# Kernel optimization log

Measured on AMD Instinct MI355X. Metric: run time of the kernel, lower is better.

Reference implementation:

```python
import jax, jax.numpy as jnp
import numpy as np

B, T, K = 512, 512, 128
START, STOP = K - 2, K - 1
NEG = -10000.0


def setup_inputs() -> dict:
    key = jax.random.key(0)
    k1, k2, k3, k4 = jax.random.split(key, 4)
    feats = jax.random.normal(k1, (B, T, K), dtype=jnp.float32)
    transitions = jax.random.normal(k2, (K, K), dtype=jnp.float32)
    # CRF.__init__ clamps transitions INTO the start tag and OUT of the stop tag
    transitions = transitions.at[START, :].set(NEG).at[:, STOP].set(NEG)
    tags = jax.random.randint(k3, (B, T), 0, K - 2, dtype=jnp.int32)
    lengths = jax.random.randint(k4, (B,), 1, T + 1, dtype=jnp.int32)
    return {"feats": feats, "transitions": transitions, "tags": tags, "lengths": lengths}


def _forward_alg(feats, trans, lengths):
    # feats: [B, T, K]
    Bb, Tt, Kk = feats.shape
    alpha0 = jnp.full((Bb, Kk), NEG, dtype=feats.dtype).at[:, START].set(0.0)

    def step(alpha, emit):
        # tag_var[b, j, k] = emit[b, j] + trans[j, k] + alpha[b, k]
        tag_var = emit[:, :, None] + trans[None, :, :] + alpha[:, None, :]
        new = jax.nn.logsumexp(tag_var, axis=2)  # stable max + log-sum-exp
        return new, new

    _, alphas = jax.lax.scan(step, alpha0, jnp.swapaxes(feats, 0, 1))  # [T, B, K]
    alphas_all = jnp.concatenate([alpha0[None], alphas], axis=0)       # [T+1, B, K]
    # pick forward_var at position lengths[b] (original indexes [b, lens_[b], :])
    fv = alphas_all[lengths, jnp.arange(Bb)]                            # [B, K]
    terminal = fv + trans[STOP][None, :]
    return jax.nn.logsumexp(terminal, axis=1)                           # [B]


def _score_sentence(feats, trans, tags, lengths):
    Bb, Tt, Kk = feats.shape
    pos = jnp.arange(Tt)
    valid = pos[None, :] < lengths[:, None]                             # [B, T]
    # pad_stop_tags: tags with positions >= len replaced by STOP, then STOP appended
    tags_stop = jnp.where(valid, tags, STOP)
    pad_stop = jnp.concatenate(
        [tags_stop, jnp.full((Bb, 1), STOP, dtype=tags.dtype)], axis=1)  # [B, T+1]
    pad_start = jnp.concatenate(
        [jnp.full((Bb, 1), START, dtype=tags.dtype), tags], axis=1)     # [B, T+1]
    trans_terms = trans[pad_stop, pad_start]                            # [B, T+1]
    tmask = jnp.arange(Tt + 1)[None, :] <= lengths[:, None]             # i in [0, len]
    tscore = jnp.sum(jnp.where(tmask, trans_terms, 0.0), axis=1)
    emit = jnp.take_along_axis(feats, tags[:, :, None].astype(jnp.int32), axis=2)[:, :, 0]
    escore = jnp.sum(jnp.where(valid, emit, 0.0), axis=1)
    return tscore + escore                                              # [B]


def reference(feats, transitions, tags, lengths):
    forward_score = _forward_alg(feats, transitions, lengths)
    gold_score = _score_sentence(feats, transitions, tags, lengths)
    return jnp.mean(jnp.abs(forward_score - gold_score))
```

## Files before the change

### kernel.cpp

```cpp
#include <hip/hip_runtime.h>
#include <math.h>

#define KK 128
#define TT 512
#define BB 512
#define TAG_START 126
#define TAG_STOP 127

typedef float v4f __attribute__((ext_vector_type(4)));

#define XI(j) ((j) + (((j) >> 5) << 2))

template <int CTRL>
__device__ __forceinline__ float dpp_movf(float x) {
    return __int_as_float(
        __builtin_amdgcn_update_dpp(0, __float_as_int(x), CTRL, 0xF, 0xF, true));
}

#define STEP_BARRIER() asm volatile("s_waitcnt lgkmcnt(0)\n\ts_barrier" ::: "memory")


__global__ __launch_bounds__(512) void order_kernel(const int* __restrict__ lengths,
                                                    int* __restrict__ order) {
    __shared__ int L[BB];
    int tid = threadIdx.x;
    L[tid] = lengths[tid];
    __syncthreads();
    int mylen = L[tid];
    int r = 0;
    for (int i = 0; i < BB; i++) {
        int li = L[i];
        r += (li > mylen) || (li == mylen && i < tid);
    }
    order[r] = tid;
}

__global__ __launch_bounds__(512, 4) void fused_kernel(
    const float* __restrict__ feats, const float* __restrict__ trans,
    const int* __restrict__ tags, const int* __restrict__ lengths,
    const int* __restrict__ order,
    float* __restrict__ fwd_out, float* __restrict__ gold_out) {
    int tid = threadIdx.x;
    int w = tid >> 6;
    int l = tid & 63;

    if (blockIdx.x < BB) {
        int b = order[blockIdx.x];

        __shared__ __align__(16) float xs[2][160];
        __shared__ float As[2];
        __shared__ float redm[8], reds[8];

        int g = (l >> 4) & 3;
        int c = l & 15;
        bool b0 = (l & 1) != 0;
        bool b1 = (l & 2) != 0;
        int row_mine = 16 * w + 4 * g + 2 * (l & 1) + ((l >> 1) & 1);
        int xoff = 8 * c + 4 * (c >> 2);
        int xw = XI(row_mine);
        bool writer = (l & 12) == 0;

        v4f tv[8];
#pragma unroll
        for (int r = 0; r < 4; r++) {
            const float* tp = trans + (16 * w + 4 * g + r) * KK + 8 * c;
            asm volatile("global_load_dwordx4 %0, %1, off"
                         : "=v"(tv[2 * r]) : "v"(tp));
            asm volatile("global_load_dwordx4 %0, %1, off"
                         : "=v"(tv[2 * r + 1]) : "v"(tp + 4));
        }
        int len = lengths[b];
        const float* fbr = feats + (size_t)b * TT * KK + row_mine;
        asm volatile("s_waitcnt vmcnt(0)"
                     : "+v"(tv[0]), "+v"(tv[1]), "+v"(tv[2]), "+v"(tv[3]),
                       "+v"(tv[4]), "+v"(tv[5]), "+v"(tv[6]), "+v"(tv[7]));

        float Mj0, Mj1, Mj2, Mj3;
        {
            float m[4];
#pragma unroll
            for (int r = 0; r < 4; r++) {
                v4f aL = tv[2 * r], aH = tv[2 * r + 1];
                float mm = fmaxf(fmaxf(fmaxf(aL.x, aL.y), fmaxf(aL.z, aL.w)),
                                 fmaxf(fmaxf(aH.x, aH.y), fmaxf(aH.z, aH.w)));
#pragma unroll
                for (int off = 1; off <= 8; off <<= 1)
                    mm = fmaxf(mm, __shfl_xor(mm, off));
                m[r] = mm;
            }
            Mj0 = m[0]; Mj1 = m[1]; Mj2 = m[2]; Mj3 = m[3];
        }
        float Mj_mine = b0 ? (b1 ? Mj3 : Mj2) : (b1 ? Mj1 : Mj0);

        float Erow[32];
#pragma unroll
        for (int r = 0; r < 4; r++) {
            float mr = (r == 0) ? Mj0 : (r == 1) ? Mj1 : (r == 2) ? Mj2 : Mj3;
            Erow[8 * r + 0] = __expf(tv[2 * r].x - mr);
            Erow[8 * r + 1] = __expf(tv[2 * r].y - mr);
            Erow[8 * r + 2] = __expf(tv[2 * r].z - mr);
            Erow[8 * r + 3] = __expf(tv[2 * r].w - mr);
            Erow[8 * r + 4] = __expf(tv[2 * r + 1].x - mr);
            Erow[8 * r + 5] = __expf(tv[2 * r + 1].y - mr);
            Erow[8 * r + 6] = __expf(tv[2 * r + 1].z - mr);
            Erow[8 * r + 7] = __expf(tv[2 * r + 1].w - mr);
        }

        if (writer) xs[0][xw] = (row_mine == TAG_START) ? 1.0f : 0.0f;
        if (tid == 0) { As[0] = 0.f; As[1] = 0.f; }

        float alpha = 0.f, A = 0.f;
        float emb[8];
#pragma unroll
        for (int d = 0; d < 8; d++) {
            int tf = (d < len) ? d : (len - 1);
            emb[d] = fbr[(size_t)tf * KK];
        }
        __syncthreads();

        int tmax = (len + 7) & ~7;
        for (int t0 = 0; t0 < tmax; t0 += 8) {
#pragma unroll
            for (int d = 0; d < 8; d++) {
                int t = t0 + d;
                if (t < len) {
                    float em = emb[d];
                    int tf = (t + 8 < len) ? (t + 8) : (len - 1);
                    emb[d] = fbr[(size_t)tf * KK];

                    int cur = t & 1, nxt = cur ^ 1;
                    float Sn = As[nxt];
                    float fac = __expf(em + Mj_mine + A - Sn);
                    const v4f* xp = (const v4f*)(xs[cur] + xoff);
                    v4f xa = xp[0], xb = xp[1];
                    float a0 = 0.f, a1 = 0.f, a2 = 0.f, a3 = 0.f;
                    a0 = fmaf(Erow[0], xa.x, a0);  a0 = fmaf(Erow[1], xa.y, a0);
                    a0 = fmaf(Erow[2], xa.z, a0);  a0 = fmaf(Erow[3], xa.w, a0);
                    a0 = fmaf(Erow[4], xb.x, a0);  a0 = fmaf(Erow[5], xb.y, a0);
                    a0 = fmaf(Erow[6], xb.z, a0);  a0 = fmaf(Erow[7], xb.w, a0);
                    a1 = fmaf(Erow[8], xa.x, a1);  a1 = fmaf(Erow[9], xa.y, a1);
                    a1 = fmaf(Erow[10], xa.z, a1); a1 = fmaf(Erow[11], xa.w, a1);
                    a1 = fmaf(Erow[12], xb.x, a1); a1 = fmaf(Erow[13], xb.y, a1);
                    a1 = fmaf(Erow[14], xb.z, a1); a1 = fmaf(Erow[15], xb.w, a1);
                    a2 = fmaf(Erow[16], xa.x, a2); a2 = fmaf(Erow[17], xa.y, a2);
                    a2 = fmaf(Erow[18], xa.z, a2); a2 = fmaf(Erow[19], xa.w, a2);
                    a2 = fmaf(Erow[20], xb.x, a2); a2 = fmaf(Erow[21], xb.y, a2);
                    a2 = fmaf(Erow[22], xb.z, a2); a2 = fmaf(Erow[23], xb.w, a2);
                    a3 = fmaf(Erow[24], xa.x, a3); a3 = fmaf(Erow[25], xa.y, a3);
                    a3 = fmaf(Erow[26], xa.z, a3); a3 = fmaf(Erow[27], xa.w, a3);
                    a3 = fmaf(Erow[28], xb.x, a3); a3 = fmaf(Erow[29], xb.y, a3);
                    a3 = fmaf(Erow[30], xb.z, a3); a3 = fmaf(Erow[31], xb.w, a3);
                    float k0 = b0 ? a2 : a0;
                    float k1 = b0 ? a3 : a1;
                    float s0 = b0 ? a0 : a2;
                    float s1 = b0 ? a1 : a3;
                    k0 += dpp_movf<0xB1>(s0);
                    k1 += dpp_movf<0xB1>(s1);
                    float kk = b1 ? k1 : k0;
                    float ss = b1 ? k0 : k1;
                    kk += dpp_movf<0x4E>(ss);
                    kk += dpp_movf<0x124>(kk);
                    kk += dpp_movf<0x128>(kk);
                    if (writer) xs[nxt][xw] = kk * fac;
                    alpha = em + Mj_mine + A + __logf(kk);
                    if (tid == 0) As[cur] = alpha;
                    A = Sn;
                    STEP_BARRIER();
                }
            }
        }

        float term = writer ? (alpha + trans[TAG_STOP * KK + row_mine]) : -1e30f;
        float m = term;
#pragma unroll
        for (int off = 32; off >= 1; off >>= 1) m = fmaxf(m, __shfl_xor(m, off));
        float s = writer ? __expf(term - m) : 0.f;
#pragma unroll
        for (int off = 32; off >= 1; off >>= 1) s += __shfl_xor(s, off);
        if (l == 0) { redm[w] = m; reds[w] = s; }
        __syncthreads();
        if (tid == 0) {
            float M2 = redm[0];
            for (int i = 1; i < 8; i++) M2 = fmaxf(M2, redm[i]);
            float S2 = 0.f;
            for (int i = 0; i < 8; i++) S2 += reds[i] * __expf(redm[i] - M2);
            fwd_out[b] = M2 + __logf(S2);
        }
    } else {
        int b = blockIdx.x - BB;
        int len = lengths[b];
        const int* tg = tags + (size_t)b * TT;
        const float* fb = feats + (size_t)b * TT * KK;
        float acc = 0.f;
        for (int i = tid; i <= len; i += 512) {
            int from = (i == 0) ? TAG_START : tg[i - 1];
            int to = (i < len) ? tg[i] : TAG_STOP;
            acc += trans[to * KK + from];
        }
        for (int t = tid; t < len; t += 512)
            acc += fb[(size_t)t * KK + tg[t]];
        __shared__ float sred[8];
#pragma unroll
        for (int off = 32; off >= 1; off >>= 1) acc += __shfl_xor(acc, off);
        if ((tid & 63) == 0) sred[tid >> 6] = acc;
        __syncthreads();
        if (tid == 0) {
            float s = 0.f;
            for (int i = 0; i < 8; i++) s += sred[i];
            gold_out[b] = s;
        }
    }
}

__global__ __launch_bounds__(512) void final_kernel(const float* __restrict__ fwd_s,
                                                    const float* __restrict__ gold_s,
                                                    float* __restrict__ out) {
    int tid = threadIdx.x;
    float v = fabsf(fwd_s[tid] - gold_s[tid]);
#pragma unroll
    for (int off = 32; off >= 1; off >>= 1) v += __shfl_xor(v, off);
    __shared__ float sred[8];
    if ((tid & 63) == 0) sred[tid >> 6] = v;
    __syncthreads();
    if (tid == 0) {
        float s = 0.f;
        for (int i = 0; i < 8; i++) s += sred[i];
        out[0] = s / (float)BB;
    }
}

extern "C" void kernel_launch(void* const* d_in, const int* in_sizes, int n_in,
                              void* d_out, int out_size, void* d_ws, size_t ws_size,
                              hipStream_t stream) {
    const float* feats = (const float*)d_in[0];
    const float* trans = (const float*)d_in[1];
    const int* tags = (const int*)d_in[2];
    const int* lengths = (const int*)d_in[3];

    float* ws = (float*)d_ws;
    float* fwdv = ws;
    float* goldv = ws + BB;
    int* order = (int*)(ws + 2 * BB);

    order_kernel<<<1, 512, 0, stream>>>(lengths, order);
    fused_kernel<<<2 * BB, 512, 0, stream>>>(feats, trans, tags, lengths, order,
                                             fwdv, goldv);
    final_kernel<<<1, 512, 0, stream>>>(fwdv, goldv, (float*)d_out);
}
```

Before: 341.1 us.

## Use persistent blocks with atomic work queue and interleaved length ordering

```diff
diff --git a/kernel.cpp b/kernel.cpp
--- a/kernel.cpp
+++ b/kernel.cpp
@@ -21,9 +21,11 @@
 
 
 __global__ __launch_bounds__(512) void order_kernel(const int* __restrict__ lengths,
-                                                    int* __restrict__ order) {
+                                                    int* __restrict__ order,
+                                                    int* __restrict__ ctr) {
     __shared__ int L[BB];
     int tid = threadIdx.x;
+    if (tid == 0) *ctr = 0;
     L[tid] = lengths[tid];
     __syncthreads();
     int mylen = L[tid];
@@ -32,182 +34,193 @@
         int li = L[i];
         r += (li > mylen) || (li == mylen && i < tid);
     }
-    order[r] = tid;
+    int task = (r < BB / 2) ? (2 * r) : (2 * (BB - 1 - r) + 1);
+    order[task] = tid;
 }
 
 __global__ __launch_bounds__(512, 4) void fused_kernel(
     const float* __restrict__ feats, const float* __restrict__ trans,
     const int* __restrict__ tags, const int* __restrict__ lengths,
-    const int* __restrict__ order,
+    const int* __restrict__ order, int* __restrict__ ctr,
     float* __restrict__ fwd_out, float* __restrict__ gold_out) {
     int tid = threadIdx.x;
     int w = tid >> 6;
     int l = tid & 63;
 
-    if (blockIdx.x < BB) {
-        int b = order[blockIdx.x];
-
-        __shared__ __align__(16) float xs[2][160];
-        __shared__ float As[2];
-        __shared__ float redm[8], reds[8];
-
-        int g = (l >> 4) & 3;
-        int c = l & 15;
-        bool b0 = (l & 1) != 0;
-        bool b1 = (l & 2) != 0;
-        int row_mine = 16 * w + 4 * g + 2 * (l & 1) + ((l >> 1) & 1);
-        int xoff = 8 * c + 4 * (c >> 2);
-        int xw = XI(row_mine);
-        bool writer = (l & 12) == 0;
-
-        v4f tv[8];
+    __shared__ __align__(16) float xs[2][160];
+    __shared__ float As[2];
+    __shared__ float redm[8], reds[8];
+    __shared__ float sred[8];
+    __shared__ int task_s;
+
+    int g = (l >> 4) & 3;
+    int c = l & 15;
+    bool b0 = (l & 1) != 0;
+    bool b1 = (l & 2) != 0;
+    int row_mine = 16 * w + 4 * g + 2 * (l & 1) + ((l >> 1) & 1);
+    int xoff = 8 * c + 4 * (c >> 2);
+    int xw = XI(row_mine);
+    bool writer = (l & 12) == 0;
+
+    v4f tv[8];
+#pragma unroll
+    for (int r = 0; r < 4; r++) {
+        const float* tp = trans + (16 * w + 4 * g + r) * KK + 8 * c;
+        asm volatile("global_load_dwordx4 %0, %1, off"
+                     : "=v"(tv[2 * r]) : "v"(tp));
+        asm volatile("global_load_dwordx4 %0, %1, off"
+                     : "=v"(tv[2 * r + 1]) : "v"(tp + 4));
+    }
+    asm volatile("s_waitcnt vmcnt(0)"
+                 : "+v"(tv[0]), "+v"(tv[1]), "+v"(tv[2]), "+v"(tv[3]),
+                   "+v"(tv[4]), "+v"(tv[5]), "+v"(tv[6]), "+v"(tv[7]));
+
+    float Mj0, Mj1, Mj2, Mj3;
+    {
+        float m[4];
 #pragma unroll
         for (int r = 0; r < 4; r++) {
-            const float* tp = trans + (16 * w + 4 * g + r) * KK + 8 * c;
-            asm volatile("global_load_dwordx4 %0, %1, off"
-                         : "=v"(tv[2 * r]) : "v"(tp));
-            asm volatile("global_load_dwordx4 %0, %1, off"
-                         : "=v"(tv[2 * r + 1]) : "v"(tp + 4));
+            v4f aL = tv[2 * r], aH = tv[2 * r + 1];
+            float mm = fmaxf(fmaxf(fmaxf(aL.x, aL.y), fmaxf(aL.z, aL.w)),
+                             fmaxf(fmaxf(aH.x, aH.y), fmaxf(aH.z, aH.w)));
+#pragma unroll
+            for (int off = 1; off <= 8; off <<= 1)
+                mm = fmaxf(mm, __shfl_xor(mm, off));
+            m[r] = mm;
         }
-        int len = lengths[b];
-        const float* fbr = feats + (size_t)b * TT * KK + row_mine;
-        asm volatile("s_waitcnt vmcnt(0)"
-                     : "+v"(tv[0]), "+v"(tv[1]), "+v"(tv[2]), "+v"(tv[3]),
-                       "+v"(tv[4]), "+v"(tv[5]), "+v"(tv[6]), "+v"(tv[7]));
-
-        float Mj0, Mj1, Mj2, Mj3;
-        {
-            float m[4];
-#pragma unroll
-            for (int r = 0; r < 4; r++) {
-                v4f aL = tv[2 * r], aH = tv[2 * r + 1];
-                float mm = fmaxf(fmaxf(fmaxf(aL.x, aL.y), fmaxf(aL.z, aL.w)),
-                                 fmaxf(fmaxf(aH.x, aH.y), fmaxf(aH.z, aH.w)));
-#pragma unroll
-                for (int off = 1; off <= 8; off <<= 1)
-                    mm = fmaxf(mm, __shfl_xor(mm, off));
-                m[r] = mm;
-            }
-            Mj0 = m[0]; Mj1 = m[1]; Mj2 = m[2]; Mj3 = m[3];
-        }
-        float Mj_mine = b0 ? (b1 ? Mj3 : Mj2) : (b1 ? Mj1 : Mj0);
-
-        float Erow[32];
-#pragma unroll
-        for (int r = 0; r < 4; r++) {
-            float mr = (r == 0) ? Mj0 : (r == 1) ? Mj1 : (r == 2) ? Mj2 : Mj3;
-            Erow[8 * r + 0] = __expf(tv[2 * r].x - mr);
-            Erow[8 * r + 1] = __expf(tv[2 * r].y - mr);
-            Erow[8 * r + 2] = __expf(tv[2 * r].z - mr);
-            Erow[8 * r + 3] = __expf(tv[2 * r].w - mr);
-            Erow[8 * r + 4] = __expf(tv[2 * r + 1].x - mr);
-            Erow[8 * r + 5] = __expf(tv[2 * r + 1].y - mr);
-            Erow[8 * r + 6] = __expf(tv[2 * r + 1].z - mr);
-            Erow[8 * r + 7] = __expf(tv[2 * r + 1].w - mr);
-        }
-
-        if (writer) xs[0][xw] = (row_mine == TAG_START) ? 1.0f : 0.0f;
-        if (tid == 0) { As[0] = 0.f; As[1] = 0.f; }
-
-        float alpha = 0.f, A = 0.f;
-        float emb[8];
-#pragma unroll
-        for (int d = 0; d < 8; d++) {
-            int tf = (d < len) ? d : (len - 1);
-            emb[d] = fbr[(size_t)tf * KK];
-        }
+        Mj0 = m[0]; Mj1 = m[1]; Mj2 = m[2]; Mj3 = m[3];
+    }
+    float Mj_mine = b0 ? (b1 ? Mj3 : Mj2) : (b1 ? Mj1 : Mj0);
+
+    float Erow[32];
+#pragma unroll
+    for (int r = 0; r < 4; r++) {
+        float mr = (r == 0) ? Mj0 : (r == 1) ? Mj1 : (r == 2) ? Mj2 : Mj3;
+        Erow[8 * r + 0] = __expf(tv[2 * r].x - mr);
+        Erow[8 * r + 1] = __expf(tv[2 * r].y - mr);
+        Erow[8 * r + 2] = __expf(tv[2 * r].z - mr);
+        Erow[8 * r + 3] = __expf(tv[2 * r].w - mr);
+        Erow[8 * r + 4] = __expf(tv[2 * r + 1].x - mr);
+        Erow[8 * r + 5] = __expf(tv[2 * r + 1].y - mr);
+        Erow[8 * r + 6] = __expf(tv[2 * r + 1].z - mr);
+        Erow[8 * r + 7] = __expf(tv[2 * r + 1].w - mr);
+    }
+
+    for (;;) {
+        if (tid == 0) task_s = atomicAdd(ctr, 1);
         __syncthreads();
-
-        int tmax = (len + 7) & ~7;
-        for (int t0 = 0; t0 < tmax; t0 += 8) {
+        int task = task_s;
+        if (task >= 2 * BB) return;
+
+        if (task < BB) {
+            int b = order[task];
+            int len = lengths[b];
+            const float* fbr = feats + (size_t)b * TT * KK + row_mine;
+
+            if (writer) xs[0][xw] = (row_mine == TAG_START) ? 1.0f : 0.0f;
+            if (tid == 0) { As[0] = 0.f; As[1] = 0.f; }
+
+            float alpha = 0.f, A = 0.f;
+            float emb[8];
 #pragma unroll
             for (int d = 0; d < 8; d++) {
-                int t = t0 + d;
-                if (t < len) {
-                    float em = emb[d];
-                    int tf = (t + 8 < len) ? (t + 8) : (len - 1);
-                    emb[d] = fbr[(size_t)tf * KK];
-
-                    int cur = t & 1, nxt = cur ^ 1;
-                    float Sn = As[nxt];
-                    float fac = __expf(em + Mj_mine + A - Sn);
-                    const v4f* xp = (const v4f*)(xs[cur] + xoff);
-                    v4f xa = xp[0], xb = xp[1];
-                    float a0 = 0.f, a1 = 0.f, a2 = 0.f, a3 = 0.f;
-                    a0 = fmaf(Erow[0], xa.x, a0);  a0 = fmaf(Erow[1], xa.y, a0);
-                    a0 = fmaf(Erow[2], xa.z, a0);  a0 = fmaf(Erow[3], xa.w, a0);
-                    a0 = fmaf(Erow[4], xb.x, a0);  a0 = fmaf(Erow[5], xb.y, a0);
-                    a0 = fmaf(Erow[6], xb.z, a0);  a0 = fmaf(Erow[7], xb.w, a0);
-                    a1 = fmaf(Erow[8], xa.x, a1);  a1 = fmaf(Erow[9], xa.y, a1);
-                    a1 = fmaf(Erow[10], xa.z, a1); a1 = fmaf(Erow[11], xa.w, a1);
-                    a1 = fmaf(Erow[12], xb.x, a1); a1 = fmaf(Erow[13], xb.y, a1);
-                    a1 = fmaf(Erow[14], xb.z, a1); a1 = fmaf(Erow[15], xb.w, a1);
-                    a2 = fmaf(Erow[16], xa.x, a2); a2 = fmaf(Erow[17], xa.y, a2);
-                    a2 = fmaf(Erow[18], xa.z, a2); a2 = fmaf(Erow[19], xa.w, a2);
-                    a2 = fmaf(Erow[20], xb.x, a2); a2 = fmaf(Erow[21], xb.y, a2);
-                    a2 = fmaf(Erow[22], xb.z, a2); a2 = fmaf(Erow[23], xb.w, a2);
-                    a3 = fmaf(Erow[24], xa.x, a3); a3 = fmaf(Erow[25], xa.y, a3);
-                    a3 = fmaf(Erow[26], xa.z, a3); a3 = fmaf(Erow[27], xa.w, a3);
-                    a3 = fmaf(Erow[28], xb.x, a3); a3 = fmaf(Erow[29], xb.y, a3);
-                    a3 = fmaf(Erow[30], xb.z, a3); a3 = fmaf(Erow[31], xb.w, a3);
-                    float k0 = b0 ? a2 : a0;
-                    float k1 = b0 ? a3 : a1;
-                    float s0 = b0 ? a0 : a2;
-                    float s1 = b0 ? a1 : a3;
-                    k0 += dpp_movf<0xB1>(s0);
-                    k1 += dpp_movf<0xB1>(s1);
-                    float kk = b1 ? k1 : k0;
-                    float ss = b1 ? k0 : k1;
-                    kk += dpp_movf<0x4E>(ss);
-                    kk += dpp_movf<0x124>(kk);
-                    kk += dpp_movf<0x128>(kk);
-                    if (writer) xs[nxt][xw] = kk * fac;
-                    alpha = em + Mj_mine + A + __logf(kk);
-                    if (tid == 0) As[cur] = alpha;
-                    A = Sn;
-                    STEP_BARRIER();
+                int tf = (d < len) ? d : (len - 1);
+                emb[d] = fbr[(size_t)tf * KK];
+            }
+            __syncthreads();
+
+            int tmax = (len + 7) & ~7;
+            for (int t0 = 0; t0 < tmax; t0 += 8) {
+#pragma unroll
+                for (int d = 0; d < 8; d++) {
+                    int t = t0 + d;
+                    if (t < len) {
+                        float em = emb[d];
+                        int tf = (t + 8 < len) ? (t + 8) : (len - 1);
+                        emb[d] = fbr[(size_t)tf * KK];
+
+                        int cur = t & 1, nxt = cur ^ 1;
+                        float Sn = As[nxt];
+                        float fac = __expf(em + Mj_mine + A - Sn);
+                        const v4f* xp = (const v4f*)(xs[cur] + xoff);
+                        v4f xa = xp[0], xb = xp[1];
+                        float a0 = 0.f, a1 = 0.f, a2 = 0.f, a3 = 0.f;
+                        a0 = fmaf(Erow[0], xa.x, a0);  a0 = fmaf(Erow[1], xa.y, a0);
+                        a0 = fmaf(Erow[2], xa.z, a0);  a0 = fmaf(Erow[3], xa.w, a0);
+                        a0 = fmaf(Erow[4], xb.x, a0);  a0 = fmaf(Erow[5], xb.y, a0);
+                        a0 = fmaf(Erow[6], xb.z, a0);  a0 = fmaf(Erow[7], xb.w, a0);
+                        a1 = fmaf(Erow[8], xa.x, a1);  a1 = fmaf(Erow[9], xa.y, a1);
+                        a1 = fmaf(Erow[10], xa.z, a1); a1 = fmaf(Erow[11], xa.w, a1);
+                        a1 = fmaf(Erow[12], xb.x, a1); a1 = fmaf(Erow[13], xb.y, a1);
+                        a1 = fmaf(Erow[14], xb.z, a1); a1 = fmaf(Erow[15], xb.w, a1);
+                        a2 = fmaf(Erow[16], xa.x, a2); a2 = fmaf(Erow[17], xa.y, a2);
+                        a2 = fmaf(Erow[18], xa.z, a2); a2 = fmaf(Erow[19], xa.w, a2);
+                        a2 = fmaf(Erow[20], xb.x, a2); a2 = fmaf(Erow[21], xb.y, a2);
+                        a2 = fmaf(Erow[22], xb.z, a2); a2 = fmaf(Erow[23], xb.w, a2);
+                        a3 = fmaf(Erow[24], xa.x, a3); a3 = fmaf(Erow[25], xa.y, a3);
+                        a3 = fmaf(Erow[26], xa.z, a3); a3 = fmaf(Erow[27], xa.w, a3);
+                        a3 = fmaf(Erow[28], xb.x, a3); a3 = fmaf(Erow[29], xb.y, a3);
+                        a3 = fmaf(Erow[30], xb.z, a3); a3 = fmaf(Erow[31], xb.w, a3);
+                        float k0 = b0 ? a2 : a0;
+                        float k1 = b0 ? a3 : a1;
+                        float s0 = b0 ? a0 : a2;
+                        float s1 = b0 ? a1 : a3;
+                        k0 += dpp_movf<0xB1>(s0);
+                        k1 += dpp_movf<0xB1>(s1);
+                        float kk = b1 ? k1 : k0;
+                        float ss = b1 ? k0 : k1;
+                        kk += dpp_movf<0x4E>(ss);
+                        kk += dpp_movf<0x124>(kk);
+                        kk += dpp_movf<0x128>(kk);
+                        if (writer) xs[nxt][xw] = kk * fac;
+                        alpha = em + Mj_mine + A + __logf(kk);
+                        if (tid == 0) As[cur] = alpha;
+                        A = Sn;
+                        STEP_BARRIER();
+                    }
                 }
             }
-        }
-
-        float term = writer ? (alpha + trans[TAG_STOP * KK + row_mine]) : -1e30f;
-        float m = term;
-#pragma unroll
-        for (int off = 32; off >= 1; off >>= 1) m = fmaxf(m, __shfl_xor(m, off));
-        float s = writer ? __expf(term - m) : 0.f;
-#pragma unroll
-        for (int off = 32; off >= 1; off >>= 1) s += __shfl_xor(s, off);
-        if (l == 0) { redm[w] = m; reds[w] = s; }
-        __syncthreads();
-        if (tid == 0) {
-            float M2 = redm[0];
-            for (int i = 1; i < 8; i++) M2 = fmaxf(M2, redm[i]);
-            float S2 = 0.f;
-            for (int i = 0; i < 8; i++) S2 += reds[i] * __expf(redm[i] - M2);
-            fwd_out[b] = M2 + __logf(S2);
-        }
-    } else {
-        int b = blockIdx.x - BB;
-        int len = lengths[b];
-        const int* tg = tags + (size_t)b * TT;
-        const float* fb = feats + (size_t)b * TT * KK;
-        float acc = 0.f;
-        for (int i = tid; i <= len; i += 512) {
-            int from = (i == 0) ? TAG_START : tg[i - 1];
-            int to = (i < len) ? tg[i] : TAG_STOP;
-            acc += trans[to * KK + from];
-        }
-        for (int t = tid; t < len; t += 512)
-            acc += fb[(size_t)t * KK + tg[t]];
-        __shared__ float sred[8];
-#pragma unroll
-        for (int off = 32; off >= 1; off >>= 1) acc += __shfl_xor(acc, off);
-        if ((tid & 63) == 0) sred[tid >> 6] = acc;
-        __syncthreads();
-        if (tid == 0) {
-            float s = 0.f;
-            for (int i = 0; i < 8; i++) s += sred[i];
-            gold_out[b] = s;
+
+            float term = writer ? (alpha + trans[TAG_STOP * KK + row_mine]) : -1e30f;
+            float m = term;
+#pragma unroll
+            for (int off = 32; off >= 1; off >>= 1) m = fmaxf(m, __shfl_xor(m, off));
+            float s = writer ? __expf(term - m) : 0.f;
+#pragma unroll
+            for (int off = 32; off >= 1; off >>= 1) s += __shfl_xor(s, off);
+            if (l == 0) { redm[w] = m; reds[w] = s; }
+            __syncthreads();
+            if (tid == 0) {
+                float M2 = redm[0];
+                for (int i = 1; i < 8; i++) M2 = fmaxf(M2, redm[i]);
+                float S2 = 0.f;
+                for (int i = 0; i < 8; i++) S2 += reds[i] * __expf(redm[i] - M2);
+                fwd_out[b] = M2 + __logf(S2);
+            }
+            __syncthreads();
+        } else {
+            int b = task - BB;
+            int len = lengths[b];
+            const int* tg = tags + (size_t)b * TT;
+            const float* fb = feats + (size_t)b * TT * KK;
+            float acc = 0.f;
+            for (int i = tid; i <= len; i += 512) {
+                int from = (i == 0) ? TAG_START : tg[i - 1];
+                int to = (i < len) ? tg[i] : TAG_STOP;
+                acc += trans[to * KK + from];
+            }
+            for (int t = tid; t < len; t += 512)
+                acc += fb[(size_t)t * KK + tg[t]];
+#pragma unroll
+            for (int off = 32; off >= 1; off >>= 1) acc += __shfl_xor(acc, off);
+            if (l == 0) sred[w] = acc;
+            __syncthreads();
+            if (tid == 0) {
+                float s = 0.f;
+                for (int i = 0; i < 8; i++) s += sred[i];
+                gold_out[b] = s;
+            }
+            __syncthreads();
         }
     }
 }
@@ -241,9 +254,10 @@
     float* fwdv = ws;
     float* goldv = ws + BB;
     int* order = (int*)(ws + 2 * BB);
-
-    order_kernel<<<1, 512, 0, stream>>>(lengths, order);
-    fused_kernel<<<2 * BB, 512, 0, stream>>>(feats, trans, tags, lengths, order,
-                                             fwdv, goldv);
+    int* ctr = (int*)d_out;
+
+    order_kernel<<<1, 512, 0, stream>>>(lengths, order, ctr);
+    fused_kernel<<<BB, 512, 0, stream>>>(feats, trans, tags, lengths, order,
+                                         ctr, fwdv, goldv);
     final_kernel<<<1, 512, 0, stream>>>(fwdv, goldv, (float*)d_out);
 }
```

After: 356.2 us. 1.04x slower.

## Process two length-sorted sequences per block to share per-step barriers

Applied to the files above, without the earlier changes.

```diff
diff --git a/kernel.cpp b/kernel.cpp
--- a/kernel.cpp
+++ b/kernel.cpp
@@ -44,11 +44,12 @@
     int w = tid >> 6;
     int l = tid & 63;
 
-    if (blockIdx.x < BB) {
-        int b = order[blockIdx.x];
-
-        __shared__ __align__(16) float xs[2][160];
-        __shared__ float As[2];
+    if (blockIdx.x < BB / 2) {
+        int b0i = order[2 * blockIdx.x];
+        int b1i = order[2 * blockIdx.x + 1];
+
+        __shared__ __align__(16) float xs[2][2][160];
+        __shared__ float As[2][2];
         __shared__ float redm[8], reds[8];
 
         int g = (l >> 4) & 3;
@@ -69,8 +70,10 @@
             asm volatile("global_load_dwordx4 %0, %1, off"
                          : "=v"(tv[2 * r + 1]) : "v"(tp + 4));
         }
-        int len = lengths[b];
-        const float* fbr = feats + (size_t)b * TT * KK + row_mine;
+        int len0 = lengths[b0i];
+        int len1 = lengths[b1i];
+        const float* fbr0 = feats + (size_t)b0i * TT * KK + row_mine;
+        const float* fbr1 = feats + (size_t)b1i * TT * KK + row_mine;
         asm volatile("s_waitcnt vmcnt(0)"
                      : "+v"(tv[0]), "+v"(tv[1]), "+v"(tv[2]), "+v"(tv[3]),
                        "+v"(tv[4]), "+v"(tv[5]), "+v"(tv[6]), "+v"(tv[7]));
@@ -106,88 +109,130 @@
             Erow[8 * r + 7] = __expf(tv[2 * r + 1].w - mr);
         }
 
-        if (writer) xs[0][xw] = (row_mine == TAG_START) ? 1.0f : 0.0f;
-        if (tid == 0) { As[0] = 0.f; As[1] = 0.f; }
-
-        float alpha = 0.f, A = 0.f;
-        float emb[8];
+        if (writer) {
+            float x0 = (row_mine == TAG_START) ? 1.0f : 0.0f;
+            xs[0][0][xw] = x0;
+            xs[1][0][xw] = x0;
+        }
+        if (tid == 0) {
+            As[0][0] = 0.f; As[0][1] = 0.f;
+            As[1][0] = 0.f; As[1][1] = 0.f;
+        }
+
+        float alpha0 = 0.f, A0 = 0.f;
+        float alpha1 = 0.f, A1 = 0.f;
+        float emb0[8], emb1[8];
 #pragma unroll
         for (int d = 0; d < 8; d++) {
-            int tf = (d < len) ? d : (len - 1);
-            emb[d] = fbr[(size_t)tf * KK];
+            int tf0 = (d < len0) ? d : (len0 - 1);
+            int tf1 = (d < len1) ? d : (len1 - 1);
+            emb0[d] = fbr0[(size_t)tf0 * KK];
+            emb1[d] = fbr1[(size_t)tf1 * KK];
         }
         __syncthreads();
 
-        int tmax = (len + 7) & ~7;
+        int tmax = (len0 + 7) & ~7;
         for (int t0 = 0; t0 < tmax; t0 += 8) {
 #pragma unroll
             for (int d = 0; d < 8; d++) {
                 int t = t0 + d;
-                if (t < len) {
-                    float em = emb[d];
-                    int tf = (t + 8 < len) ? (t + 8) : (len - 1);
-                    emb[d] = fbr[(size_t)tf * KK];
+                if (t < len0) {
+                    float em0 = emb0[d];
+                    int tf0 = (t + 8 < len0) ? (t + 8) : (len0 - 1);
+                    emb0[d] = fbr0[(size_t)tf0 * KK];
+                    float em1 = emb1[d];
+                    int tf1 = (t + 8 < len1) ? (t + 8) : (len1 - 1);
+                    emb1[d] = fbr1[(size_t)tf1 * KK];
+                    bool run1 = t < len1;
 
                     int cur = t & 1, nxt = cur ^ 1;
-                    float Sn = As[nxt];
-                    float fac = __expf(em + Mj_mine + A - Sn);
-                    const v4f* xp = (const v4f*)(xs[cur] + xoff);
-                    v4f xa = xp[0], xb = xp[1];
-                    float a0 = 0.f, a1 = 0.f, a2 = 0.f, a3 = 0.f;
-                    a0 = fmaf(Erow[0], xa.x, a0);  a0 = fmaf(Erow[1], xa.y, a0);
-                    a0 = fmaf(Erow[2], xa.z, a0);  a0 = fmaf(Erow[3], xa.w, a0);
-                    a0 = fmaf(Erow[4], xb.x, a0);  a0 = fmaf(Erow[5], xb.y, a0);
-                    a0 = fmaf(Erow[6], xb.z, a0);  a0 = fmaf(Erow[7], xb.w, a0);
-                    a1 = fmaf(Erow[8], xa.x, a1);  a1 = fmaf(Erow[9], xa.y, a1);
-                    a1 = fmaf(Erow[10], xa.z, a1); a1 = fmaf(Erow[11], xa.w, a1);
-                    a1 = fmaf(Erow[12], xb.x, a1); a1 = fmaf(Erow[13], xb.y, a1);
-                    a1 = fmaf(Erow[14], xb.z, a1); a1 = fmaf(Erow[15], xb.w, a1);
-                    a2 = fmaf(Erow[16], xa.x, a2); a2 = fmaf(Erow[17], xa.y, a2);
-                    a2 = fmaf(Erow[18], xa.z, a2); a2 = fmaf(Erow[19], xa.w, a2);
-                    a2 = fmaf(Erow[20], xb.x, a2); a2 = fmaf(Erow[21], xb.y, a2);
-                    a2 = fmaf(Erow[22], xb.z, a2); a2 = fmaf(Erow[23], xb.w, a2);
-                    a3 = fmaf(Erow[24], xa.x, a3); a3 = fmaf(Erow[25], xa.y, a3);
-                    a3 = fmaf(Erow[26], xa.z, a3); a3 = fmaf(Erow[27], xa.w, a3);
-                    a3 = fmaf(Erow[28], xb.x, a3); a3 = fmaf(Erow[29], xb.y, a3);
-                    a3 = fmaf(Erow[30], xb.z, a3); a3 = fmaf(Erow[31], xb.w, a3);
-                    float k0 = b0 ? a2 : a0;
-                    float k1 = b0 ? a3 : a1;
-                    float s0 = b0 ? a0 : a2;
-                    float s1 = b0 ? a1 : a3;
-                    k0 += dpp_movf<0xB1>(s0);
-                    k1 += dpp_movf<0xB1>(s1);
-                    float kk = b1 ? k1 : k0;
-                    float ss = b1 ? k0 : k1;
-                    kk += dpp_movf<0x4E>(ss);
-                    kk += dpp_movf<0x124>(kk);
-                    kk += dpp_movf<0x128>(kk);
-                    if (writer) xs[nxt][xw] = kk * fac;
-                    alpha = em + Mj_mine + A + __logf(kk);
-                    if (tid == 0) As[cur] = alpha;
-                    A = Sn;
+                    float Sn0 = As[0][nxt];
+                    float Sn1 = As[1][nxt];
+                    float fac0 = __expf(em0 + Mj_mine + A0 - Sn0);
+                    float fac1 = __expf(em1 + Mj_mine + A1 - Sn1);
+                    const v4f* xp0 = (const v4f*)(xs[0][cur] + xoff);
+                    const v4f* xp1 = (const v4f*)(xs[1][cur] + xoff);
+                    v4f xA[2], xB[2];
+                    xA[0] = xp0[0]; xB[0] = xp0[1];
+                    xA[1] = xp1[0]; xB[1] = xp1[1];
+
+                    float acc[2][4];
+#pragma unroll
+                    for (int s = 0; s < 2; s++) {
+#pragma unroll
+                        for (int r = 0; r < 4; r++) {
+                            float a = 0.f;
+                            a = fmaf(Erow[8 * r + 0], xA[s].x, a);
+                            a = fmaf(Erow[8 * r + 1], xA[s].y, a);
+                            a = fmaf(Erow[8 * r + 2], xA[s].z, a);
+                            a = fmaf(Erow[8 * r + 3], xA[s].w, a);
+                            a = fmaf(Erow[8 * r + 4], xB[s].x, a);
+                            a = fmaf(Erow[8 * r + 5], xB[s].y, a);
+                            a = fmaf(Erow[8 * r + 6], xB[s].z, a);
+                            a = fmaf(Erow[8 * r + 7], xB[s].w, a);
+                            acc[s][r] = a;
+                        }
+                    }
+                    float kk[2];
+#pragma unroll
+                    for (int s = 0; s < 2; s++) {
+                        float k0 = b0 ? acc[s][2] : acc[s][0];
+                        float k1 = b0 ? acc[s][3] : acc[s][1];
+                        float s0 = b0 ? acc[s][0] : acc[s][2];
+                        float s1 = b0 ? acc[s][1] : acc[s][3];
+                        k0 += dpp_movf<0xB1>(s0);
+                        k1 += dpp_movf<0xB1>(s1);
+                        float km = b1 ? k1 : k0;
+                        float sm = b1 ? k0 : k1;
+                        km += dpp_movf<0x4E>(sm);
+                        km += dpp_movf<0x124>(km);
+                        km += dpp_movf<0x128>(km);
+                        kk[s] = km;
+                    }
+                    if (writer) {
+                        xs[0][nxt][xw] = kk[0] * fac0;
+                        if (run1) xs[1][nxt][xw] = kk[1] * fac1;
+                    }
+                    alpha0 = em0 + Mj_mine + A0 + __logf(kk[0]);
+                    A0 = Sn0;
+                    if (run1) {
+                        alpha1 = em1 + Mj_mine + A1 + __logf(kk[1]);
+                        A1 = Sn1;
+                    }
+                    if (tid == 0) {
+                        As[0][cur] = alpha0;
+                        if (run1) As[1][cur] = alpha1;
+                    }
                     STEP_BARRIER();
                 }
             }
         }
 
-        float term = writer ? (alpha + trans[TAG_STOP * KK + row_mine]) : -1e30f;
-        float m = term;
-#pragma unroll
-        for (int off = 32; off >= 1; off >>= 1) m = fmaxf(m, __shfl_xor(m, off));
-        float s = writer ? __expf(term - m) : 0.f;
-#pragma unroll
-        for (int off = 32; off >= 1; off >>= 1) s += __shfl_xor(s, off);
-        if (l == 0) { redm[w] = m; reds[w] = s; }
-        __syncthreads();
-        if (tid == 0) {
-            float M2 = redm[0];
-            for (int i = 1; i < 8; i++) M2 = fmaxf(M2, redm[i]);
-            float S2 = 0.f;
-            for (int i = 0; i < 8; i++) S2 += reds[i] * __expf(redm[i] - M2);
-            fwd_out[b] = M2 + __logf(S2);
+        float tstop = trans[TAG_STOP * KK + row_mine];
+#pragma unroll
+        for (int s = 0; s < 2; s++) {
+            float alf = s ? alpha1 : alpha0;
+            int bs = s ? b1i : b0i;
+            float term = writer ? (alf + tstop) : -1e30f;
+            float m = term;
+#pragma unroll
+            for (int off = 32; off >= 1; off >>= 1) m = fmaxf(m, __shfl_xor(m, off));
+            float sv = writer ? __expf(term - m) : 0.f;
+#pragma unroll
+            for (int off = 32; off >= 1; off >>= 1) sv += __shfl_xor(sv, off);
+            if (l == 0) { redm[w] = m; reds[w] = sv; }
+            __syncthreads();
+            if (tid == 0) {
+                float M2 = redm[0];
+                for (int i = 1; i < 8; i++) M2 = fmaxf(M2, redm[i]);
+                float S2 = 0.f;
+                for (int i = 0; i < 8; i++) S2 += reds[i] * __expf(redm[i] - M2);
+                fwd_out[bs] = M2 + __logf(S2);
+            }
+            __syncthreads();
         }
     } else {
-        int b = blockIdx.x - BB;
+        int b = blockIdx.x - BB / 2;
         int len = lengths[b];
         const int* tg = tags + (size_t)b * TT;
         const float* fb = feats + (size_t)b * TT * KK;
@@ -243,7 +288,7 @@
     int* order = (int*)(ws + 2 * BB);
 
     order_kernel<<<1, 512, 0, stream>>>(lengths, order);
-    fused_kernel<<<2 * BB, 512, 0, stream>>>(feats, trans, tags, lengths, order,
-                                             fwdv, goldv);
+    fused_kernel<<<BB / 2 + BB, 512, 0, stream>>>(feats, trans, tags, lengths,
+                                                  order, fwdv, goldv);
     final_kernel<<<1, 512, 0, stream>>>(fwdv, goldv, (float*)d_out);
 }
```

Result: slower. 432.2 us (+26.7%).
